# Optimization experiments

Hardware: AMD Instinct MI355X
Metric: run time of the kernel (lower is better)

## Reference

```python
import jax, jax.numpy as jnp
import numpy as np

B, T, N, F_, H, C, E = 8, 16, 1024, 128, 8, 32, 32768
D = H * C  # 256 = hidden_channels * num_heads
NEG_SLOPE = 0.2


def setup_inputs() -> dict:
    key = jax.random.key(0)
    ks = jax.random.split(key, 16)
    p = lambda k, shape: (jax.random.normal(k, shape, jnp.float32) * 0.05)
    inp = {
        "x": jax.random.normal(ks[0], (B, T, N, F_), jnp.float32),
        "edge_index": jax.random.randint(ks[1], (2, E), 0, N, jnp.int64),
        "edge_weight": jax.random.uniform(ks[2], (E,), jnp.float32),
        # GAT layer 1
        "W1": p(ks[3], (F_, D)), "att_src1": p(ks[4], (H, C)),
        "att_dst1": p(ks[5], (H, C)), "b1": jnp.zeros((D,), jnp.float32),
        # GAT layer 2
        "W2": p(ks[6], (D, D)), "att_src2": p(ks[7], (H, C)),
        "att_dst2": p(ks[8], (H, C)), "b2": jnp.zeros((D,), jnp.float32),
        # LSTM (torch gate order: i, f, g, o)
        "lstm_Wih": p(ks[9], (4 * D, D)), "lstm_Whh": p(ks[10], (4 * D, D)),
        "lstm_bih": jnp.zeros((4 * D,), jnp.float32),
        "lstm_bhh": jnp.zeros((4 * D,), jnp.float32),
        # edge predictors
        "Wp": p(ks[11], (1, D)), "bp": jnp.zeros((1,), jnp.float32),
        "Wc": p(ks[12], (1, D)), "bc": jnp.zeros((1,), jnp.float32),
    }
    return inp


def _gat_layer(x2d, src, dst, W, a_src, a_dst, b):
    # x2d: [N, Fin]; src/dst: [Et] (self-loops already appended)
    h = (x2d @ W).reshape(N, H, C)              # [N, H, C]
    es = jnp.sum(h * a_src, axis=-1)            # [N, H]
    ed = jnp.sum(h * a_dst, axis=-1)            # [N, H]
    e = jax.nn.leaky_relu(es[src] + ed[dst], NEG_SLOPE)  # [Et, H]
    m = jax.ops.segment_max(e, dst, num_segments=N)      # [N, H]
    m = jnp.where(jnp.isfinite(m), m, 0.0)
    pnum = jnp.exp(e - m[dst])                  # [Et, H]
    denom = jax.ops.segment_sum(pnum, dst, num_segments=N)
    alpha = pnum / (denom[dst] + 1e-16)         # segment softmax over incoming edges
    out = jax.ops.segment_sum(alpha[:, :, None] * h[src], dst, num_segments=N)
    return out.reshape(N, D) + b                # concat heads + bias


def _forward(x, edge_index, edge_weight, W1, att_src1, att_dst1, b1,
             W2, att_src2, att_dst2, b2, lstm_Wih, lstm_Whh, lstm_bih,
             lstm_bhh, Wp, bp, Wc, bc):
    # GATConv ignores edge_weight when edge_dim is None (lin_edge is None).
    sl = jnp.arange(N, dtype=edge_index.dtype)
    src = jnp.concatenate([edge_index[0], sl])  # add_self_loops=True
    dst = jnp.concatenate([edge_index[1], sl])

    def per_graph(xi):  # xi: [N, F_]
        hh = jax.nn.relu(_gat_layer(xi, src, dst, W1, att_src1, att_dst1, b1))
        hh = jax.nn.relu(_gat_layer(hh, src, dst, W2, att_src2, att_dst2, b2))
        return hh  # [N, D]

    # stack timesteps then batches == reshape to [B*T, N, F_]
    hall = jax.vmap(per_graph)(x.reshape(B * T, N, F_))  # [B*T, N, D]

    # LSTM over the node dimension (batch_first=True, batch=B*T, seq=N)
    def step(carry, xt):
        hprev, cprev = carry
        z = xt @ lstm_Wih.T + hprev @ lstm_Whh.T + lstm_bih + lstm_bhh
        i, f, g, o = jnp.split(z, 4, axis=-1)
        c = jax.nn.sigmoid(f) * cprev + jax.nn.sigmoid(i) * jnp.tanh(g)
        hcur = jax.nn.sigmoid(o) * jnp.tanh(c)
        return (hcur, hcur * 0 + c)[0:1] * 0 or ((hcur, c), hcur)

    def step2(carry, xt):
        hprev, cprev = carry
        z = xt @ lstm_Wih.T + hprev @ lstm_Whh.T + lstm_bih + lstm_bhh
        i, f, g, o = jnp.split(z, 4, axis=-1)
        c = jax.nn.sigmoid(f) * cprev + jax.nn.sigmoid(i) * jnp.tanh(g)
        hcur = jax.nn.sigmoid(o) * jnp.tanh(c)
        return (hcur, c), hcur

    init = (jnp.zeros((B * T, D), hall.dtype), jnp.zeros((B * T, D), hall.dtype))
    _, hs = jax.lax.scan(step2, init, jnp.swapaxes(hall, 0, 1))  # [N, B*T, D]
    out = jnp.swapaxes(hs, 0, 1)      # [B*T, N, D]

    xsel = out[::T]                   # [B, N, D]
    xflat = xsel.reshape(B * N, D)
    xe = xflat[edge_index[0]] * xflat[edge_index[1]]  # [E, D]
    edge_weights_pred = xe @ Wp.T + bp                # [E, 1]
    logits = (xe @ Wc.T + bc).squeeze(-1)             # [E]
    return edge_weights_pred, logits


def reference(x, edge_index, edge_weight, W1, att_src1, att_dst1, b1,
              W2, att_src2, att_dst2, b2, lstm_Wih, lstm_Whh, lstm_bih,
              lstm_bhh, Wp, bp, Wc, bc):
    return _forward(x, edge_index, edge_weight, W1, att_src1, att_dst1, b1,
                    W2, att_src2, att_dst2, b2, lstm_Wih, lstm_Whh, lstm_bih,
                    lstm_bhh, Wp, bp, Wc, bc)
```

## Files before the change

kernel.cpp:

```cpp
#include <hip/hip_runtime.h>
#include <math.h>

#define NN 1024
#define FF 128
#define DD 256
#define HH 8
#define CC 32
#define EE 32768
#define NEDGE (EE + NN)

typedef unsigned int u32x2 __attribute__((ext_vector_type(2)));

__device__ __forceinline__ float sigf(float x) { return 1.0f / (1.0f + expf(-x)); }
__device__ __forceinline__ float fsig(float x) { return 1.0f / (1.0f + __expf(-x)); }
__device__ __forceinline__ float ftanh(float x) { return 2.0f / (1.0f + __expf(-2.0f * x)) - 1.0f; }

__device__ __forceinline__ void store_l2_u64(unsigned long long* p, unsigned long long v) {
  asm volatile("global_store_dwordx2 %0, %1, off sc0" :: "v"(p), "v"(v) : "memory");
}
__device__ __forceinline__ u32x2 load_l2_u64(const unsigned long long* p) {
  u32x2 r;
  asm volatile("global_load_dwordx2 %0, %1, off sc0\n\ts_waitcnt vmcnt(0)"
               : "=v"(r) : "v"(p) : "memory");
  return r;
}

__global__ void k_count(const int* __restrict__ ei, int* __restrict__ count) {
  int k = blockIdx.x * blockDim.x + threadIdx.x;
  if (k >= NEDGE) return;
  int d = (k < EE) ? ei[EE + k] : (k - EE);
  atomicAdd(&count[d], 1);
}

__global__ void k_scan(const int* __restrict__ count, int* __restrict__ rowptr, int* __restrict__ cursor) {
  __shared__ int buf[NN];
  int t = threadIdx.x;
  int c = count[t];
  buf[t] = c;
  __syncthreads();
  for (int off = 1; off < NN; off <<= 1) {
    int add = (t >= off) ? buf[t - off] : 0;
    __syncthreads();
    buf[t] += add;
    __syncthreads();
  }
  int inc = buf[t];
  rowptr[t] = inc - c;
  cursor[t] = inc - c;
  if (t == NN - 1) rowptr[NN] = inc;
}

__global__ void k_scatter(const int* __restrict__ ei, int* __restrict__ cursor, int* __restrict__ csrc) {
  int k = blockIdx.x * blockDim.x + threadIdx.x;
  if (k >= NEDGE) return;
  int s, d;
  if (k < EE) { s = ei[k]; d = ei[EE + k]; }
  else        { s = k - EE; d = k - EE; }
  int pos = atomicAdd(&cursor[d], 1);
  csrc[pos] = s;
}

template<bool BT, bool ADDB>
__global__ __launch_bounds__(256) void k_gemm(const float* __restrict__ A, const float* __restrict__ B,
    const float* __restrict__ bias1, const float* __restrict__ bias2, float* __restrict__ C,
    int M, int N, int K) {
  __shared__ float At[64][17];
  __shared__ float Bt[16][65];
  const int tid = threadIdx.x;
  const int m0 = blockIdx.x * 64, n0 = blockIdx.y * 64;
  const int tx = tid & 15, ty = tid >> 4;
  float acc[4][4] = {{0.f, 0.f, 0.f, 0.f}};
  for (int k0 = 0; k0 < K; k0 += 16) {
    {
      int rr = tid >> 2, kl = (tid & 3) * 4;
      float4 a = *(const float4*)(A + (m0 + rr) * K + k0 + kl);
      At[rr][kl] = a.x; At[rr][kl + 1] = a.y; At[rr][kl + 2] = a.z; At[rr][kl + 3] = a.w;
    }
    if (BT) {
      int nn = tid >> 2, kl = (tid & 3) * 4;
      float4 b = *(const float4*)(B + (n0 + nn) * K + k0 + kl);
      Bt[kl][nn] = b.x; Bt[kl + 1][nn] = b.y; Bt[kl + 2][nn] = b.z; Bt[kl + 3][nn] = b.w;
    } else {
      int kk = tid >> 4, nn = (tid & 15) * 4;
      float4 b = *(const float4*)(B + (k0 + kk) * N + n0 + nn);
      Bt[kk][nn] = b.x; Bt[kk][nn + 1] = b.y; Bt[kk][nn + 2] = b.z; Bt[kk][nn + 3] = b.w;
    }
    __syncthreads();
    #pragma unroll
    for (int kk = 0; kk < 16; ++kk) {
      float av[4], bv[4];
      #pragma unroll
      for (int i = 0; i < 4; ++i) av[i] = At[ty * 4 + i][kk];
      #pragma unroll
      for (int jj = 0; jj < 4; ++jj) bv[jj] = Bt[kk][tx * 4 + jj];
      #pragma unroll
      for (int i = 0; i < 4; ++i)
        #pragma unroll
        for (int jj = 0; jj < 4; ++jj)
          acc[i][jj] = fmaf(av[i], bv[jj], acc[i][jj]);
    }
    __syncthreads();
  }
  #pragma unroll
  for (int i = 0; i < 4; ++i) {
    #pragma unroll
    for (int jj = 0; jj < 4; ++jj) {
      int n = n0 + tx * 4 + jj;
      float v = acc[i][jj];
      if (ADDB) v += bias1[n] + bias2[n];
      C[(m0 + ty * 4 + i) * N + n] = v;
    }
  }
}

__global__ __launch_bounds__(256) void k_att(const float* __restrict__ h, const float* __restrict__ asrc,
    const float* __restrict__ adst, float* __restrict__ es, float* __restrict__ ed) {
  int n = blockIdx.x;
  int hd = threadIdx.x >> 5, c = threadIdx.x & 31;
  float hv = h[n * DD + hd * CC + c];
  float e1 = hv * asrc[hd * CC + c];
  float e2 = hv * adst[hd * CC + c];
  #pragma unroll
  for (int msk = 1; msk < 32; msk <<= 1) { e1 += __shfl_xor(e1, msk); e2 += __shfl_xor(e2, msk); }
  if (c == 0) { es[n * HH + hd] = e1; ed[n * HH + hd] = e2; }
}

__global__ __launch_bounds__(256) void k_agg(const float* __restrict__ h, const float* __restrict__ es,
    const float* __restrict__ ed, const float* __restrict__ bias, const int* __restrict__ rowptr,
    const int* __restrict__ csrc, float* __restrict__ out) {
  int w = blockIdx.x * 4 + (threadIdx.x >> 6);
  int lane = threadIdx.x & 63;
  int n = w >> 3, hd = w & 7;
  int lo = rowptr[n], hi = rowptr[n + 1];
  float edn = ed[n * HH + hd];
  float m = -1e30f;
  for (int k = lo + lane; k < hi; k += 64) {
    int s = csrc[k];
    float e = es[s * HH + hd] + edn;
    e = (e > 0.f) ? e : 0.2f * e;
    m = fmaxf(m, e);
  }
  #pragma unroll
  for (int msk = 1; msk < 64; msk <<= 1) m = fmaxf(m, __shfl_xor(m, msk));
  float den = 0.f;
  for (int k = lo + lane; k < hi; k += 64) {
    int s = csrc[k];
    float e = es[s * HH + hd] + edn;
    e = (e > 0.f) ? e : 0.2f * e;
    den += expf(e - m);
  }
  #pragma unroll
  for (int msk = 1; msk < 64; msk <<= 1) den += __shfl_xor(den, msk);
  float inv = 1.0f / (den + 1e-16f);
  int c = lane & 31, halfsel = lane >> 5;
  float acc = 0.f;
  for (int k = lo + halfsel; k < hi; k += 2) {
    int s = csrc[k];
    float e = es[s * HH + hd] + edn;
    e = (e > 0.f) ? e : 0.2f * e;
    float al = expf(e - m) * inv;
    acc += al * h[s * DD + hd * CC + c];
  }
  acc += __shfl_down(acc, 32);
  if (lane < 32) {
    float v = acc + bias[hd * CC + c];
    out[n * DD + hd * CC + c] = fmaxf(v, 0.f);
  }
}

__global__ __launch_bounds__(512, 1) void k_lstm(const float* __restrict__ xW,
    const float* __restrict__ Whh, unsigned long long* __restrict__ fastw,
    unsigned long long* __restrict__ sloww, float* __restrict__ hs) {
  const int bid = blockIdx.x;
  const int coh = bid & 7;
  const int j = bid >> 3;
  unsigned long long* fw = fastw + coh * 2 * DD;
  unsigned long long* sw = sloww + coh * 2 * DD;
  const int t = threadIdx.x;
  const int r = t >> 2, qt = t & 3;
  const int g = r >> 5, kl = r & 31;
  const int grow = g * 256 + j * 32 + kl;
  __shared__ float hlds[DD];
  __shared__ float zlds[128];

  float4 w[16];
  {
    const float4* W4 = (const float4*)(Whh + grow * DD + qt * 64);
    #pragma unroll
    for (int q = 0; q < 16; ++q)
      asm volatile("global_load_dwordx4 %0, %1, off" : "=v"(w[q]) : "v"(W4 + q));
    asm volatile("s_waitcnt vmcnt(0)" ::: "memory");
  }
  if (t < DD) hlds[t] = 0.f;
  float creg = 0.f;
  float xwv = xW[grow];
  int ftries = 64, lateMiss = 0;
  int bud = 1 << 24;
  __syncthreads();

  for (int s = 0; s < NN; ++s) {
    const float4* h4 = ((const float4*)hlds) + qt * 16;
    float ac4[4] = {0.f, 0.f, 0.f, 0.f};
    #pragma unroll
    for (int q = 0; q < 16; ++q) {
      float4 hv = h4[q];
      ac4[q & 3] = fmaf(w[q].x, hv.x, ac4[q & 3]);
      ac4[q & 3] = fmaf(w[q].y, hv.y, ac4[q & 3]);
      ac4[q & 3] = fmaf(w[q].z, hv.z, ac4[q & 3]);
      ac4[q & 3] = fmaf(w[q].w, hv.w, ac4[q & 3]);
    }
    float acc = (ac4[0] + ac4[1]) + (ac4[2] + ac4[3]);
    acc += __shfl_xor(acc, 1);
    acc += __shfl_xor(acc, 2);
    if (qt == 0) zlds[r] = acc + xwv;
    __syncthreads();

    const int par = (s + 1) & 1;
    const unsigned int tag = (unsigned int)(s + 1);
    float xw_next = (s + 1 < NN) ? xW[(s + 1) * 1024 + grow] : 0.f;

    if (t < 32) {
      float iv = zlds[t], fv = zlds[32 + t], gv = zlds[64 + t], ov = zlds[96 + t];
      creg = fsig(fv) * creg + fsig(iv) * ftanh(gv);
      float hn = fsig(ov) * ftanh(creg);
      int col = j * 32 + t;
      hlds[col] = hn;
      unsigned long long pk = ((unsigned long long)__float_as_uint(hn) << 32) | tag;
      store_l2_u64(&fw[par * DD + col], pk);
      __hip_atomic_store(&sw[par * DD + col], pk, __ATOMIC_RELAXED, __HIP_MEMORY_SCOPE_AGENT);
      hs[s * DD + col] = hn;
    } else if (t >= 64 && t < 288) {
      int pi = t - 64;
      int peer = j + 1 + (pi >> 5); if (peer >= 8) peer -= 8;
      int col = peer * 32 + (pi & 31);
      int idx = par * DD + col;
      u32x2 v; bool got = false;
      for (int tr = 0; tr < ftries; ++tr) {
        v = load_l2_u64(&fw[idx]);
        if (v.x == tag) { got = true; break; }
      }
      if (!got) {
        if (s >= 4) ++lateMiss;
        if (lateMiss >= 8 && ftries > 2) ftries = 2;
        unsigned long long a;
        for (;;) {
          a = __hip_atomic_load(&sw[idx], __ATOMIC_RELAXED, __HIP_MEMORY_SCOPE_AGENT);
          if ((unsigned int)(a & 0xffffffffULL) == tag) break;
          if (--bud <= 0) break;
          __builtin_amdgcn_s_sleep(1);
        }
        v.y = (unsigned int)(a >> 32);
      }
      hlds[col] = __uint_as_float(v.y);
    }
    __syncthreads();
    xwv = xw_next;
  }
}

__global__ __launch_bounds__(256) void k_edges(const float* __restrict__ hs, const int* __restrict__ ei,
    const float* __restrict__ Wp, const float* __restrict__ bp,
    const float* __restrict__ Wc, const float* __restrict__ bc, float* __restrict__ out) {
  int widx = threadIdx.x >> 6, lane = threadIdx.x & 63;
  int k = blockIdx.x * 4 + widx;
  int sIdx = ei[k], dIdx = ei[EE + k];
  float4 u = ((const float4*)(hs + sIdx * DD))[lane];
  float4 v = ((const float4*)(hs + dIdx * DD))[lane];
  float4 wp = ((const float4*)Wp)[lane];
  float4 wc = ((const float4*)Wc)[lane];
  float x0 = u.x * v.x, x1 = u.y * v.y, x2 = u.z * v.z, x3 = u.w * v.w;
  float ap = x0 * wp.x + x1 * wp.y + x2 * wp.z + x3 * wp.w;
  float ac = x0 * wc.x + x1 * wc.y + x2 * wc.z + x3 * wc.w;
  #pragma unroll
  for (int msk = 1; msk < 64; msk <<= 1) { ap += __shfl_xor(ap, msk); ac += __shfl_xor(ac, msk); }
  if (lane == 0) { out[k] = ap + bp[0]; out[EE + k] = ac + bc[0]; }
}

extern "C" void kernel_launch(void* const* d_in, const int* in_sizes, int n_in,
                              void* d_out, int out_size, void* d_ws, size_t ws_size,
                              hipStream_t stream) {
  const float* x       = (const float*)d_in[0];
  const int* ei        = (const int*)d_in[1];
  const float* W1      = (const float*)d_in[3];
  const float* as1     = (const float*)d_in[4];
  const float* ad1     = (const float*)d_in[5];
  const float* b1      = (const float*)d_in[6];
  const float* W2      = (const float*)d_in[7];
  const float* as2     = (const float*)d_in[8];
  const float* ad2     = (const float*)d_in[9];
  const float* b2      = (const float*)d_in[10];
  const float* Wih     = (const float*)d_in[11];
  const float* Whh     = (const float*)d_in[12];
  const float* bih     = (const float*)d_in[13];
  const float* bhh     = (const float*)d_in[14];
  const float* Wp      = (const float*)d_in[15];
  const float* bp      = (const float*)d_in[16];
  const float* Wc      = (const float*)d_in[17];
  const float* bc      = (const float*)d_in[18];
  float* out = (float*)d_out;

  char* ws = (char*)d_ws;
  int* counts                = (int*)(ws + 0);
  unsigned long long* fastw  = (unsigned long long*)(ws + 4096);
  unsigned long long* sloww  = (unsigned long long*)(ws + 36864);
  int* rowptr                = (int*)(ws + 69632);
  int* cursor                = (int*)(ws + 77824);
  int* csrc                  = (int*)(ws + 81920);
  float* es                  = (float*)(ws + 221184);
  float* ed                  = (float*)(ws + 253952);
  float* buf0                = (float*)(ws + 286720);
  float* buf1                = (float*)(ws + 1335296);
  float* xW                  = (float*)(ws + 2383872);
  float* hsall               = (float*)(ws + 6578176);

  hipMemsetAsync(ws, 0, 69632, stream);

  k_count  <<<(NEDGE + 255) / 256, 256, 0, stream>>>(ei, counts);
  k_scan   <<<1, 1024, 0, stream>>>(counts, rowptr, cursor);
  k_scatter<<<(NEDGE + 255) / 256, 256, 0, stream>>>(ei, cursor, csrc);

  k_gemm<false, false><<<dim3(16, 4), 256, 0, stream>>>(x, W1, nullptr, nullptr, buf0, NN, DD, FF);
  k_att<<<NN, 256, 0, stream>>>(buf0, as1, ad1, es, ed);
  k_agg<<<NN * HH / 4, 256, 0, stream>>>(buf0, es, ed, b1, rowptr, csrc, buf1);

  k_gemm<false, false><<<dim3(16, 4), 256, 0, stream>>>(buf1, W2, nullptr, nullptr, buf0, NN, DD, DD);
  k_att<<<NN, 256, 0, stream>>>(buf0, as2, ad2, es, ed);
  k_agg<<<NN * HH / 4, 256, 0, stream>>>(buf0, es, ed, b2, rowptr, csrc, buf1);

  k_gemm<true, true><<<dim3(16, 16), 256, 0, stream>>>(buf1, Wih, bih, bhh, xW, NN, 1024, DD);

  k_lstm<<<64, 512, 0, stream>>>(xW, Whh, fastw, sloww, hsall);

  k_edges<<<EE / 4, 256, 0, stream>>>(hsall, ei, Wp, bp, Wc, bc, out);
}
```

Before: 2.156 ms.

## Hold LSTM recurrent weights in AGPRs, rotate LDS reads, lighten barriers

Moves the per-thread Whh slice from VGPRs into accumulation registers (AGPRs), read back with v_accvgpr_read before each FMA. It rotates the LDS read order per quarter-thread so the four threads of a row hit different banks. It also replaces __syncthreads with a barrier that waits only on LDS counters, and loads xW only in the lane that consumes it. The aim is lower register pressure and less LDS conflict and sync cost in the serial recurrence, at the cost of extra AGPR read instructions and a smaller spin budget in the fallback wait.

```diff
diff --git a/kernel.cpp b/kernel.cpp
--- a/kernel.cpp
+++ b/kernel.cpp
@@ -23,6 +23,12 @@
   asm volatile("global_load_dwordx2 %0, %1, off sc0\n\ts_waitcnt vmcnt(0)"
                : "=v"(r) : "v"(p) : "memory");
   return r;
+}
+
+__device__ __forceinline__ void barrier_lds() {
+  asm volatile("s_waitcnt lgkmcnt(0)" ::: "memory");
+  __builtin_amdgcn_sched_barrier(0);
+  __builtin_amdgcn_s_barrier();
 }
 
 __global__ void k_count(const int* __restrict__ ei, int* __restrict__ count) {
@@ -183,41 +189,52 @@
   __shared__ float hlds[DD];
   __shared__ float zlds[128];
 
-  float4 w[16];
+  float wa[64];
   {
     const float4* W4 = (const float4*)(Whh + grow * DD + qt * 64);
     #pragma unroll
-    for (int q = 0; q < 16; ++q)
-      asm volatile("global_load_dwordx4 %0, %1, off" : "=v"(w[q]) : "v"(W4 + q));
-    asm volatile("s_waitcnt vmcnt(0)" ::: "memory");
+    for (int q = 0; q < 16; ++q) {
+      const int qp = (q + 4 * qt) & 15;
+      float4 tmp = W4[qp];
+      asm volatile("v_accvgpr_write_b32 %0, %1" : "=a"(wa[4 * q + 0]) : "v"(tmp.x));
+      asm volatile("v_accvgpr_write_b32 %0, %1" : "=a"(wa[4 * q + 1]) : "v"(tmp.y));
+      asm volatile("v_accvgpr_write_b32 %0, %1" : "=a"(wa[4 * q + 2]) : "v"(tmp.z));
+      asm volatile("v_accvgpr_write_b32 %0, %1" : "=a"(wa[4 * q + 3]) : "v"(tmp.w));
+    }
   }
   if (t < DD) hlds[t] = 0.f;
   float creg = 0.f;
-  float xwv = xW[grow];
+  float xwv = (qt == 0) ? xW[grow] : 0.f;
   int ftries = 64, lateMiss = 0;
-  int bud = 1 << 24;
+  int bud = 1 << 20;
   __syncthreads();
 
   for (int s = 0; s < NN; ++s) {
-    const float4* h4 = ((const float4*)hlds) + qt * 16;
+    const float4* h4 = (const float4*)hlds + qt * 16;
     float ac4[4] = {0.f, 0.f, 0.f, 0.f};
     #pragma unroll
     for (int q = 0; q < 16; ++q) {
-      float4 hv = h4[q];
-      ac4[q & 3] = fmaf(w[q].x, hv.x, ac4[q & 3]);
-      ac4[q & 3] = fmaf(w[q].y, hv.y, ac4[q & 3]);
-      ac4[q & 3] = fmaf(w[q].z, hv.z, ac4[q & 3]);
-      ac4[q & 3] = fmaf(w[q].w, hv.w, ac4[q & 3]);
+      const int qp = (q + 4 * qt) & 15;
+      float4 hv = h4[qp];
+      float w0, w1, w2, w3;
+      asm volatile("v_accvgpr_read_b32 %0, %1" : "=v"(w0) : "a"(wa[4 * q + 0]));
+      asm volatile("v_accvgpr_read_b32 %0, %1" : "=v"(w1) : "a"(wa[4 * q + 1]));
+      asm volatile("v_accvgpr_read_b32 %0, %1" : "=v"(w2) : "a"(wa[4 * q + 2]));
+      asm volatile("v_accvgpr_read_b32 %0, %1" : "=v"(w3) : "a"(wa[4 * q + 3]));
+      ac4[q & 3] = fmaf(w0, hv.x, ac4[q & 3]);
+      ac4[q & 3] = fmaf(w1, hv.y, ac4[q & 3]);
+      ac4[q & 3] = fmaf(w2, hv.z, ac4[q & 3]);
+      ac4[q & 3] = fmaf(w3, hv.w, ac4[q & 3]);
     }
     float acc = (ac4[0] + ac4[1]) + (ac4[2] + ac4[3]);
     acc += __shfl_xor(acc, 1);
     acc += __shfl_xor(acc, 2);
     if (qt == 0) zlds[r] = acc + xwv;
-    __syncthreads();
+    barrier_lds();
 
     const int par = (s + 1) & 1;
     const unsigned int tag = (unsigned int)(s + 1);
-    float xw_next = (s + 1 < NN) ? xW[(s + 1) * 1024 + grow] : 0.f;
+    float xw_next = (qt == 0 && s + 1 < NN) ? xW[(s + 1) * 1024 + grow] : 0.f;
 
     if (t < 32) {
       float iv = zlds[t], fv = zlds[32 + t], gv = zlds[64 + t], ov = zlds[96 + t];
@@ -253,7 +270,7 @@
       }
       hlds[col] = __uint_as_float(v.y);
     }
-    __syncthreads();
+    barrier_lds();
     xwv = xw_next;
   }
 }
```

New measurement: 1.892 ms. -12.2%, faster.
